# Kernel optimization log

Measured on AMD Instinct MI355X. Metric: run time of the kernel, lower is better.

Reference implementation:

```python
import jax, jax.numpy as jnp
import numpy as np

B, N, D, H, C = 8, 1024, 1024, 8, 1
S = 32            # sqrt(D // C): per-patch spatial map side
HD = D // H       # head dim = 128
SCALE = HD ** -0.5
BN_EPS = 1e-3     # Keras BatchNormalization default epsilon


def setup_inputs() -> dict:
    key = jax.random.key(0)
    ks = jax.random.split(key, 7)
    std = 0.02  # matches tf.random_normal_initializer(0.0, 0.02)
    return {
        "x": jax.random.normal(ks[0], (B, N, D), jnp.float32),
        "qw": jax.random.normal(ks[1], (3, 3, C, C), jnp.float32) * std,
        "kw": jax.random.normal(ks[2], (3, 3, C, C), jnp.float32) * std,
        "vw": jax.random.normal(ks[3], (3, 3, C, C), jnp.float32) * std,
        "reatten_w": jax.random.normal(ks[4], (N, N), jnp.float32) / np.float32(np.sqrt(N)),
        "reatten_b": jnp.zeros((N,), jnp.float32),
        "bn_gamma": jnp.ones((N,), jnp.float32),
        "bn_beta": jnp.zeros((N,), jnp.float32),
        "proj_w": jax.random.normal(ks[5], (D, D), jnp.float32) / np.float32(np.sqrt(D)),
        "proj_b": jnp.zeros((D,), jnp.float32),
    }


def _conv_qkv(x, w):
    # unflatten: [B, N, D] -> [B*N, S, S, C]; map_fn over batch with a shared
    # conv == one conv with B*N as batch dim. 3x3 SAME, no bias, exact GELU.
    xm = x.reshape(B * N, S, S, C)
    y = jax.lax.conv_general_dilated(
        xm, w, window_strides=(1, 1), padding='SAME',
        dimension_numbers=('NHWC', 'HWIO', 'NHWC'))
    y = jax.nn.gelu(y, approximate=False)
    # reshape to heads: [B, N, H, HD] -> [B, H, N, HD]
    return y.reshape(B, N, H, HD).transpose(0, 2, 1, 3)


def reference(x, qw, kw, vw, reatten_w, reatten_b, bn_gamma, bn_beta, proj_w, proj_b):
    q = _conv_qkv(x, qw)
    k = _conv_qkv(x, kw)
    v = _conv_qkv(x, vw)

    attn = jax.nn.softmax(jnp.einsum('bhid,bhjd->bhij', q, k) * SCALE, axis=-1)
    # re-attention: 1x1 conv over last (key) axis + BN (inference: mean=0, var=1)
    attn = jnp.einsum('bhic,cj->bhij', attn, reatten_w) + reatten_b
    attn = attn * (bn_gamma / jnp.sqrt(jnp.float32(1.0) + BN_EPS)) + bn_beta
    # reatten_scale = 1.0 (transform_scale=False)

    out = jnp.einsum('bhij,bhjd->bhid', attn, v)
    out = out.transpose(0, 2, 1, 3).reshape(B, N, D)
    out = out @ proj_w + proj_b
    return (out, attn)
```

## Files before the change

kernel.cpp:

```cpp
#include <hip/hip_runtime.h>
#include <hip/hip_bf16.h>

typedef __attribute__((ext_vector_type(8))) short short8;
typedef __attribute__((ext_vector_type(4))) float f32x4;

__device__ __forceinline__ void gload_lds16(const void* g, void* l) {
    __builtin_amdgcn_global_load_lds(
        (const __attribute__((address_space(1))) void*)g,
        (__attribute__((address_space(3))) void*)l, 16, 0, 0);
}

__device__ __forceinline__ float gelu_exact(float x) {
    return 0.5f * x * (1.0f + erff(x * 0.70710678118654752f));
}
__device__ __forceinline__ unsigned short f2b_raw(float f) {
    __hip_bfloat16 h = __float2bfloat16(f);
    return *reinterpret_cast<unsigned short*>(&h);
}
__device__ __forceinline__ float tofloat(float f) { return f; }
__device__ __forceinline__ float tofloat(__hip_bfloat16 h) { return __bfloat162float(h); }

__global__ __launch_bounds__(256) void conv_qkv(
    const float* __restrict__ x,
    const float* __restrict__ qw, const float* __restrict__ kw, const float* __restrict__ vw,
    __hip_bfloat16* __restrict__ qb, __hip_bfloat16* __restrict__ kb, __hip_bfloat16* __restrict__ vb)
{
    __shared__ float img[1024];
    const int bid = blockIdx.x;
    const int b = bid >> 10, n = bid & 1023;
    const float* xr = x + (long)bid * 1024;
    for (int i = threadIdx.x; i < 1024; i += 256) img[i] = xr[i];
    __syncthreads();

    float wq[9], wk[9], wv[9];
    #pragma unroll
    for (int i = 0; i < 9; ++i) { wq[i] = qw[i]; wk[i] = kw[i]; wv[i] = vw[i]; }

    for (int q = 0; q < 4; ++q) {
        const int p = q * 256 + threadIdx.x;
        const int r = p >> 5, c = p & 31;
        float sq = 0.f, sk = 0.f, sv = 0.f;
        #pragma unroll
        for (int dy = 0; dy < 3; ++dy) {
            const int rr = r + dy - 1;
            if (rr < 0 || rr > 31) continue;
            #pragma unroll
            for (int dx = 0; dx < 3; ++dx) {
                const int cc = c + dx - 1;
                if (cc < 0 || cc > 31) continue;
                const float px = img[rr * 32 + cc];
                sq += px * wq[dy * 3 + dx];
                sk += px * wk[dy * 3 + dx];
                sv += px * wv[dy * 3 + dx];
            }
        }
        sq = gelu_exact(sq); sk = gelu_exact(sk); sv = gelu_exact(sv);
        const int h = p >> 7, d = p & 127;
        const long off = ((long)(b * 8 + h) * 1024 + n) * 128 + d;
        qb[off] = __float2bfloat16(sq);
        kb[off] = __float2bfloat16(sk);
        vb[off] = __float2bfloat16(sv);
    }
}

template <typename Tin>
__global__ __launch_bounds__(256) void transpose_cast(
    const Tin* __restrict__ in, __hip_bfloat16* __restrict__ out,
    int R, int Cc, long inz, long outz)
{
    __shared__ float tile[32][33];
    const long z = blockIdx.z;
    const int c0 = blockIdx.x * 32, r0 = blockIdx.y * 32;
    const int tx = threadIdx.x & 31, ty = threadIdx.x >> 5;
    const Tin* ip = in + z * inz;
    #pragma unroll
    for (int i = 0; i < 32; i += 8)
        tile[ty + i][tx] = tofloat(ip[(long)(r0 + ty + i) * Cc + (c0 + tx)]);
    __syncthreads();
    __hip_bfloat16* op = out + z * outz;
    #pragma unroll
    for (int i = 0; i < 32; i += 8)
        op[(long)(c0 + ty + i) * R + (r0 + tx)] = __float2bfloat16(tile[tx][ty + i]);
}

__global__ __launch_bounds__(256, 2) void qk_softmax(
    const __hip_bfloat16* __restrict__ qb, const __hip_bfloat16* __restrict__ kb,
    __hip_bfloat16* __restrict__ Pun, float* __restrict__ linv)
{
    __shared__ __align__(16) char smem[74240];
    char* As = smem;
    char* Bs = smem + 32768;
    __hip_bfloat16* pbuf = (__hip_bfloat16*)(smem + 65536);
    float* lred = (float*)(smem + 65536);

    const int tid = threadIdx.x;
    const int rt = blockIdx.x, z = blockIdx.y;
    const char* Ag = (const char*)(qb + ((long)z * 1024 + rt * 128) * 128);
    const char* Bg = (const char*)(kb + (long)z * 1024 * 128);

    int gsrc[8], pphys[8];
    #pragma unroll
    for (int i = 0; i < 8; ++i) {
        const int p = i * 4096 + tid * 16;
        const int L = p ^ (((p >> 8) & 7) << 4);
        pphys[i] = p; gsrc[i] = L;
    }
    auto STAGE = [&](const char* gb, char* lb) {
        #pragma unroll
        for (int i = 0; i < 8; ++i) gload_lds16(gb + gsrc[i], lb + pphys[i]);
    };
    auto LD8 = [&](const char* buf, int L) -> short8 {
        const int ph = L ^ (((L >> 8) & 7) << 4);
        return *(const short8*)(buf + ph);
    };

    const int lane = tid & 63, wave = tid >> 6;
    const int wr = (wave >> 1) * 64, wc = (wave & 1) * 64;
    const int fr = lane & 15, kl = lane >> 4;

    STAGE(Ag, As);
    STAGE(Bg, Bs);
    __syncthreads();

    short8 af[4][4];
    #pragma unroll
    for (int m = 0; m < 4; ++m)
        #pragma unroll
        for (int kk = 0; kk < 4; ++kk)
            af[m][kk] = LD8(As, (wr + m * 16 + fr) * 256 + (kl * 8 + kk * 32) * 2);

    float lacc[4][4];
    #pragma unroll
    for (int m = 0; m < 4; ++m)
        #pragma unroll
        for (int r = 0; r < 4; ++r) lacc[m][r] = 0.f;

    const float SCALE = 0.08838834764831843f;

    for (int c = 0; c < 8; ++c) {
        f32x4 acc[4][4];
        #pragma unroll
        for (int m = 0; m < 4; ++m)
            #pragma unroll
            for (int n = 0; n < 4; ++n) acc[m][n] = (f32x4){0.f, 0.f, 0.f, 0.f};

        #pragma unroll
        for (int kk = 0; kk < 4; ++kk) {
            short8 bf[4];
            #pragma unroll
            for (int n = 0; n < 4; ++n)
                bf[n] = LD8(Bs, (wc + n * 16 + fr) * 256 + (kl * 8 + kk * 32) * 2);
            #pragma unroll
            for (int m = 0; m < 4; ++m)
                #pragma unroll
                for (int n = 0; n < 4; ++n)
                    acc[m][n] = __builtin_amdgcn_mfma_f32_16x16x32_bf16(af[m][kk], bf[n], acc[m][n], 0, 0, 0);
        }

        #pragma unroll
        for (int m = 0; m < 4; ++m) {
            #pragma unroll
            for (int n = 0; n < 4; ++n)
                #pragma unroll
                for (int r = 0; r < 4; ++r)
                    acc[m][n][r] = __expf(acc[m][n][r] * SCALE);
            #pragma unroll
            for (int r = 0; r < 4; ++r)
                lacc[m][r] += (acc[m][0][r] + acc[m][1][r]) + (acc[m][2][r] + acc[m][3][r]);
        }

        #pragma unroll
        for (int q2 = 0; q2 < 4; ++q2) {
            if ((wave >> 1) == (q2 >> 1)) {
                #pragma unroll
                for (int mm = 0; mm < 2; ++mm) {
                    const int m = (q2 & 1) * 2 + mm;
                    const int lr0 = m * 16 + kl * 4 - (q2 & 1) * 32;
                    #pragma unroll
                    for (int n = 0; n < 4; ++n)
                        #pragma unroll
                        for (int r = 0; r < 4; ++r)
                            pbuf[(lr0 + r) * 136 + wc + n * 16 + fr] = __float2bfloat16(acc[m][n][r]);
                }
            }
            __syncthreads();
            #pragma unroll
            for (int p = 0; p < 2; ++p) {
                const int idx = (tid + p * 256) * 8;
                const int row = idx >> 7, col = idx & 127;
                short8 s = *(const short8*)&pbuf[row * 136 + col];
                __builtin_nontemporal_store(s,
                    (short8*)&Pun[((long)z * 1024 + rt * 128 + q2 * 32 + row) * 1024 + c * 128 + col]);
            }
            __syncthreads();
        }

        if (c < 7) {
            STAGE(Bg + (c + 1) * 32768, Bs);
            __syncthreads();
        }
    }

    #pragma unroll
    for (int m = 0; m < 4; ++m)
        #pragma unroll
        for (int r = 0; r < 4; ++r) {
            float v = lacc[m][r];
            v += __shfl_xor(v, 1); v += __shfl_xor(v, 2);
            v += __shfl_xor(v, 4); v += __shfl_xor(v, 8);
            lacc[m][r] = v;
        }
    __syncthreads();
    if (fr == 0) {
        #pragma unroll
        for (int m = 0; m < 4; ++m)
            #pragma unroll
            for (int r = 0; r < 4; ++r)
                lred[(wr + m * 16 + kl * 4 + r) * 2 + (wave & 1)] = lacc[m][r];
    }
    __syncthreads();
    if (tid < 128) {
        const float s = lred[tid * 2] + lred[tid * 2 + 1];
        linv[(long)z * 1024 + rt * 128 + tid] = 1.0f / s;
    }
}

__global__ __launch_bounds__(512, 2) void gemm_reatten_256(
    const __hip_bfloat16* __restrict__ Sall, const __hip_bfloat16* __restrict__ Wt,
    float* __restrict__ Cout, __hip_bfloat16* __restrict__ C2out,
    const float* __restrict__ bg, const float* __restrict__ rb, const float* __restrict__ bb,
    const float* __restrict__ linv)
{
    __shared__ __align__(16) char smem[131072];
    char* ldsA = smem;
    char* ldsB = smem + 65536;

    const int tid = threadIdx.x;
    const int z = blockIdx.z, tileM = blockIdx.x, tileN = blockIdx.y;
    const char* Ab = (const char*)(Sall + (long)z * 1048576 + (long)tileM * 256 * 1024);
    const char* Bb = (const char*)(Wt + (long)tileN * 256 * 1024);

    int grow[2], goff[2], pphys[2];
    #pragma unroll
    for (int i = 0; i < 2; ++i) {
        const int p = i * 8192 + tid * 16;
        const int l = p ^ (((p >> 7) & 3) << 4);
        pphys[i] = p; grow[i] = l >> 6; goff[i] = l & 63;
    }
    auto STAGE = [&](const char* gb, char* lb, int kt) {
        #pragma unroll
        for (int i = 0; i < 2; ++i)
            gload_lds16(gb + (long)grow[i] * 2048 + kt * 64 + goff[i], lb + pphys[i]);
    };

    const int lane = tid & 63, wid = tid >> 6;
    const int wrM = wid >> 2, wcn = wid & 3;
    const int fr = lane & 15, kl = lane >> 4;
    const int frbase = fr * 64 + kl * 16;

    auto LD8 = [&](const char* buf, int L) -> short8 {
        const int ph = L ^ (((L >> 7) & 3) << 4);
        return *(const short8*)(buf + ph);
    };

    f32x4 acc[8][4];
    #pragma unroll
    for (int m = 0; m < 8; ++m)
        #pragma unroll
        for (int n = 0; n < 4; ++n) acc[m][n] = (f32x4){0.f, 0.f, 0.f, 0.f};

    STAGE(Ab, ldsA, 0);          STAGE(Bb, ldsB, 0);
    STAGE(Ab, ldsA + 16384, 1);  STAGE(Bb, ldsB + 16384, 1);
    asm volatile("s_waitcnt vmcnt(4)" ::: "memory");
    __builtin_amdgcn_sched_barrier(0);
    __builtin_amdgcn_s_barrier();
    __builtin_amdgcn_sched_barrier(0);

    #pragma unroll 1
    for (int t = 0; t < 32; ++t) {
        char* bufA = ldsA + (t & 3) * 16384;
        char* bufB = ldsB + (t & 3) * 16384;
        const int t2 = t + 2;
        char* nA = ldsA + (t2 & 3) * 16384;
        char* nB = ldsB + (t2 & 3) * 16384;

        short8 bf[4], af[4], ag[4];
        #pragma unroll
        for (int n = 0; n < 4; ++n) bf[n] = LD8(bufB, ((wcn * 64 + n * 16) * 64) + frbase);
        #pragma unroll
        for (int j = 0; j < 4; ++j) af[j] = LD8(bufA, ((wrM * 128 + j * 16) * 64) + frbase);
        if (t2 < 32) STAGE(Ab, nA, t2);
        __builtin_amdgcn_s_setprio(1);
        #pragma unroll
        for (int j = 0; j < 4; ++j)
            #pragma unroll
            for (int n = 0; n < 4; ++n)
                acc[j][n] = __builtin_amdgcn_mfma_f32_16x16x32_bf16(af[j], bf[n], acc[j][n], 0, 0, 0);
        __builtin_amdgcn_s_setprio(0);

        #pragma unroll
        for (int j = 0; j < 4; ++j) ag[j] = LD8(bufA, ((wrM * 128 + 64 + j * 16) * 64) + frbase);
        if (t2 < 32) STAGE(Bb, nB, t2);
        __builtin_amdgcn_s_setprio(1);
        #pragma unroll
        for (int j = 0; j < 4; ++j)
            #pragma unroll
            for (int n = 0; n < 4; ++n)
                acc[4 + j][n] = __builtin_amdgcn_mfma_f32_16x16x32_bf16(ag[j], bf[n], acc[4 + j][n], 0, 0, 0);
        __builtin_amdgcn_s_setprio(0);

        if (t < 30)       { asm volatile("s_waitcnt vmcnt(4)" ::: "memory"); }
        else if (t == 30) { asm volatile("s_waitcnt vmcnt(0)" ::: "memory"); }
        __builtin_amdgcn_sched_barrier(0);
        __builtin_amdgcn_s_barrier();
        __builtin_amdgcn_sched_barrier(0);
    }

    __syncthreads();
    float* cbuf = (float*)smem;
    const float bninv = rsqrtf(1.0f + 1e-3f);
    float alpha[4], addv[4];
    #pragma unroll
    for (int n = 0; n < 4; ++n) {
        const int col = tileN * 256 + wcn * 64 + n * 16 + fr;
        const float g = bg[col];
        alpha[n] = g * bninv;
        addv[n] = rb[col] * alpha[n] + bb[col];
    }
    const float* linvz = linv + (long)z * 1024 + tileM * 256 + wrM * 128 + kl * 4;
    f32x4 lr[8];
    #pragma unroll
    for (int mf = 0; mf < 8; ++mf) lr[mf] = *(const f32x4*)(linvz + mf * 16);

    const int srow = tid >> 3, cseg = (tid & 7) * 4, c8 = (tid & 7) * 8;
    #pragma unroll
    for (int c = 0; c < 4; ++c) {
        if (wrM == (c >> 1)) {
            #pragma unroll
            for (int j = 0; j < 4; ++j) {
                const int mf = (c & 1) * 4 + j;
                const int lrow0 = j * 16 + kl * 4;
                #pragma unroll
                for (int n = 0; n < 4; ++n)
                    #pragma unroll
                    for (int r = 0; r < 4; ++r)
                        cbuf[(lrow0 + r) * 260 + wcn * 64 + n * 16 + fr] =
                            acc[mf][n][r] * (lr[mf][r] * alpha[n]) + addv[n];
            }
        }
        __syncthreads();
        const long gro = (long)(tileM * 256 + c * 64 + srow);
        float* gp = Cout + (long)z * 1048576 + gro * 1024 + tileN * 256;
        #pragma unroll
        for (int i = 0; i < 8; ++i) {
            f32x4 v = *(const f32x4*)&cbuf[srow * 260 + cseg + i * 32];
            __builtin_nontemporal_store(v, (f32x4*)(gp + cseg + i * 32));
        }
        __hip_bfloat16* gp2 = C2out + (long)z * 1048576 + gro * 1024 + tileN * 256;
        #pragma unroll
        for (int i = 0; i < 4; ++i) {
            const float* src = &cbuf[srow * 260 + c8 + i * 64];
            f32x4 v0 = *(const f32x4*)src;
            f32x4 v1 = *(const f32x4*)(src + 4);
            short8 s;
            #pragma unroll
            for (int k = 0; k < 4; ++k) {
                s[k] = (short)f2b_raw(v0[k]);
                s[k + 4] = (short)f2b_raw(v1[k]);
            }
            *(short8*)(gp2 + c8 + i * 64) = s;
        }
        __syncthreads();
    }
}

template <int MODE>
__global__ __launch_bounds__(256) void gemm_nt(
    const __hip_bfloat16* __restrict__ Aall, const __hip_bfloat16* __restrict__ Ball,
    void* __restrict__ Call, int K,
    long sAz, long sBz, long sCz,
    const float* __restrict__ e0)
{
    constexpr bool OF32 = (MODE == 3);

    __shared__ __align__(16) char smem[32 * 132 * 4];
    short* As = (short*)smem;
    short* Bs = (short*)(smem + 8192);
    float* cbuf = (float*)smem;

    const int tid = threadIdx.x;
    const int z = blockIdx.z;
    const int tileM = blockIdx.x, tileN = blockIdx.y;

    const short* Aw = (const short*)Aall + sAz * z + (long)tileM * 128 * K;
    const short* Bw = (const short*)Ball + sBz * z + (long)tileN * 128 * K;

    const int r0s = tid >> 2, k0s = (tid & 3) * 8;
    const int r1s = r0s + 64;

    f32x4 acc[4][4];
    #pragma unroll
    for (int m = 0; m < 4; ++m)
        #pragma unroll
        for (int n = 0; n < 4; ++n) acc[m][n] = (f32x4){0.f, 0.f, 0.f, 0.f};

    const int lane = tid & 63;
    const int wave = tid >> 6;
    const int wr = (wave >> 1) * 64, wc = (wave & 1) * 64;
    const int fr = lane & 15;
    const int kb = (lane >> 4) * 8;

    const int nk = K >> 5;
    for (int kt = 0; kt < nk; ++kt) {
        __syncthreads();
        gload_lds16(Aw + (long)r0s * K + kt * 32 + k0s, &As[tid * 8]);
        gload_lds16(Aw + (long)r1s * K + kt * 32 + k0s, &As[(tid + 256) * 8]);
        gload_lds16(Bw + (long)r0s * K + kt * 32 + k0s, &Bs[tid * 8]);
        gload_lds16(Bw + (long)r1s * K + kt * 32 + k0s, &Bs[(tid + 256) * 8]);
        __syncthreads();

        short8 af[4], bf[4];
        #pragma unroll
        for (int m = 0; m < 4; ++m) af[m] = *(const short8*)&As[(wr + m * 16 + fr) * 32 + kb];
        #pragma unroll
        for (int n = 0; n < 4; ++n) bf[n] = *(const short8*)&Bs[(wc + n * 16 + fr) * 32 + kb];
        #pragma unroll
        for (int m = 0; m < 4; ++m)
            #pragma unroll
            for (int n = 0; n < 4; ++n)
                acc[m][n] = __builtin_amdgcn_mfma_f32_16x16x32_bf16(af[m], bf[n], acc[m][n], 0, 0, 0);
    }

    long cbase;
    if (MODE == 2) cbase = (long)(z >> 3) * 1048576 + (long)(z & 7) * 128;
    else           cbase = sCz * z;

    float addv[4];
    #pragma unroll
    for (int n = 0; n < 4; ++n) {
        const int col = tileN * 128 + wc + n * 16 + fr;
        addv[n] = (MODE == 3) ? e0[col] : 0.f;
    }

    __syncthreads();
    #pragma unroll
    for (int q = 0; q < 4; ++q) {
        if ((wave >> 1) == (q >> 1)) {
            #pragma unroll
            for (int mm = 0; mm < 2; ++mm) {
                const int m = (q & 1) * 2 + mm;
                const int lr0 = m * 16 + (lane >> 4) * 4 - (q & 1) * 32;
                #pragma unroll
                for (int n = 0; n < 4; ++n)
                    #pragma unroll
                    for (int r = 0; r < 4; ++r)
                        cbuf[(lr0 + r) * 132 + wc + n * 16 + fr] = acc[m][n][r] + addv[n];
            }
        }
        __syncthreads();
        const long growbase = (long)tileM * 128 + q * 32;
        if constexpr (OF32) {
            float* Cg = (float*)Call + cbase;
            #pragma unroll
            for (int pass = 0; pass < 4; ++pass) {
                const int idx = (tid + pass * 256) * 4;
                const int row = idx >> 7, col = idx & 127;
                f32x4 v = *(const f32x4*)&cbuf[row * 132 + col];
                __builtin_nontemporal_store(v,
                    (f32x4*)&Cg[(growbase + row) * 1024 + tileN * 128 + col]);
            }
        } else {
            __hip_bfloat16* Cg = (__hip_bfloat16*)Call + cbase;
            #pragma unroll
            for (int pass = 0; pass < 2; ++pass) {
                const int idx = (tid + pass * 256) * 8;
                const int row = idx >> 7, col = idx & 127;
                const float* src = &cbuf[row * 132 + col];
                f32x4 v0 = *(const f32x4*)src;
                f32x4 v1 = *(const f32x4*)(src + 4);
                short8 s;
                #pragma unroll
                for (int i = 0; i < 4; ++i) {
                    s[i] = (short)f2b_raw(v0[i]);
                    s[i + 4] = (short)f2b_raw(v1[i]);
                }
                *(short8*)&Cg[(growbase + row) * 1024 + tileN * 128 + col] = s;
            }
        }
        __syncthreads();
    }
}

extern "C" void kernel_launch(void* const* d_in, const int* in_sizes, int n_in,
                              void* d_out, int out_size, void* d_ws, size_t ws_size,
                              hipStream_t stream)
{
    const float* x  = (const float*)d_in[0];
    const float* qw = (const float*)d_in[1];
    const float* kw = (const float*)d_in[2];
    const float* vw = (const float*)d_in[3];
    const float* rw = (const float*)d_in[4];
    const float* rb = (const float*)d_in[5];
    const float* bg = (const float*)d_in[6];
    const float* bb = (const float*)d_in[7];
    const float* pw = (const float*)d_in[8];
    const float* pb = (const float*)d_in[9];

    float* outF  = (float*)d_out;
    float* attnF = outF + 8388608;

    char* w = (char*)d_ws;
    __hip_bfloat16* qb    = (__hip_bfloat16*)w; w += 16777216;
    __hip_bfloat16* kb    = (__hip_bfloat16*)w; w += 16777216;
    __hip_bfloat16* vb    = (__hip_bfloat16*)w; w += 16777216;
    __hip_bfloat16* vt    = (__hip_bfloat16*)w; w += 16777216;
    __hip_bfloat16* Wt    = (__hip_bfloat16*)w; w += 2097152;
    __hip_bfloat16* pWt   = (__hip_bfloat16*)w; w += 2097152;
    __hip_bfloat16* o2    = (__hip_bfloat16*)w; w += 16777216;
    float*          linv  = (float*)w;          w += 262144;
    __hip_bfloat16* Pun   = (__hip_bfloat16*)w; w += 134217728;
    __hip_bfloat16* attnb = (__hip_bfloat16*)w; w += 134217728;

    conv_qkv<<<8192, 256, 0, stream>>>(x, qw, kw, vw, qb, kb, vb);
    transpose_cast<float><<<dim3(32, 32, 1), 256, 0, stream>>>(rw, Wt, 1024, 1024, 0, 0);
    transpose_cast<float><<<dim3(32, 32, 1), 256, 0, stream>>>(pw, pWt, 1024, 1024, 0, 0);
    transpose_cast<__hip_bfloat16><<<dim3(4, 32, 64), 256, 0, stream>>>(vb, vt, 1024, 128, 131072, 131072);

    qk_softmax<<<dim3(8, 64), 256, 0, stream>>>(qb, kb, Pun, linv);
    gemm_reatten_256<<<dim3(4, 4, 64), 512, 0, stream>>>(Pun, Wt, attnF, attnb, bg, rb, bb, linv);
    gemm_nt<2><<<dim3(8, 1, 64), 256, 0, stream>>>(
        attnb, vt, o2, 1024, 1048576, 131072, 0, nullptr);
    gemm_nt<3><<<dim3(64, 8, 1), 256, 0, stream>>>(
        o2, pWt, outF, 1024, 0, 0, 0, pb);
}
```

Before: 371.9 us.

## Drop bf16 attention copy; attn@V GEMM reads fp32 attn and converts in-kernel

```diff
diff --git a/kernel.cpp b/kernel.cpp
--- a/kernel.cpp
+++ b/kernel.cpp
@@ -184,6 +184,7 @@
                 }
             }
             __syncthreads();
+            if (q2 == 0 && c < 7) STAGE(Bg + (c + 1) * 32768, Bs);
             #pragma unroll
             for (int p = 0; p < 2; ++p) {
                 const int idx = (tid + p * 256) * 8;
@@ -194,11 +195,6 @@
             }
             __syncthreads();
         }
-
-        if (c < 7) {
-            STAGE(Bg + (c + 1) * 32768, Bs);
-            __syncthreads();
-        }
     }
 
     #pragma unroll
@@ -227,7 +223,7 @@
 
 __global__ __launch_bounds__(512, 2) void gemm_reatten_256(
     const __hip_bfloat16* __restrict__ Sall, const __hip_bfloat16* __restrict__ Wt,
-    float* __restrict__ Cout, __hip_bfloat16* __restrict__ C2out,
+    float* __restrict__ Cout,
     const float* __restrict__ bg, const float* __restrict__ rb, const float* __restrict__ bb,
     const float* __restrict__ linv)
 {
@@ -332,7 +328,7 @@
     #pragma unroll
     for (int mf = 0; mf < 8; ++mf) lr[mf] = *(const f32x4*)(linvz + mf * 16);
 
-    const int srow = tid >> 3, cseg = (tid & 7) * 4, c8 = (tid & 7) * 8;
+    const int srow = tid >> 3, cseg = (tid & 7) * 4;
     #pragma unroll
     for (int c = 0; c < 4; ++c) {
         if (wrM == (c >> 1)) {
@@ -356,31 +352,18 @@
             f32x4 v = *(const f32x4*)&cbuf[srow * 260 + cseg + i * 32];
             __builtin_nontemporal_store(v, (f32x4*)(gp + cseg + i * 32));
         }
-        __hip_bfloat16* gp2 = C2out + (long)z * 1048576 + gro * 1024 + tileN * 256;
-        #pragma unroll
-        for (int i = 0; i < 4; ++i) {
-            const float* src = &cbuf[srow * 260 + c8 + i * 64];
-            f32x4 v0 = *(const f32x4*)src;
-            f32x4 v1 = *(const f32x4*)(src + 4);
-            short8 s;
-            #pragma unroll
-            for (int k = 0; k < 4; ++k) {
-                s[k] = (short)f2b_raw(v0[k]);
-                s[k + 4] = (short)f2b_raw(v1[k]);
-            }
-            *(short8*)(gp2 + c8 + i * 64) = s;
-        }
         __syncthreads();
     }
 }
 
 template <int MODE>
 __global__ __launch_bounds__(256) void gemm_nt(
-    const __hip_bfloat16* __restrict__ Aall, const __hip_bfloat16* __restrict__ Ball,
+    const void* __restrict__ Aall, const __hip_bfloat16* __restrict__ Ball,
     void* __restrict__ Call, int K,
     long sAz, long sBz, long sCz,
     const float* __restrict__ e0)
 {
+    constexpr bool AF32 = (MODE == 2);
     constexpr bool OF32 = (MODE == 3);
 
     __shared__ __align__(16) char smem[32 * 132 * 4];
@@ -392,7 +375,10 @@
     const int z = blockIdx.z;
     const int tileM = blockIdx.x, tileN = blockIdx.y;
 
-    const short* Aw = (const short*)Aall + sAz * z + (long)tileM * 128 * K;
+    const short* AwB = nullptr;
+    const float* AwF = nullptr;
+    if constexpr (AF32) AwF = (const float*)Aall + sAz * z + (long)tileM * 128 * K;
+    else                AwB = (const short*)Aall + sAz * z + (long)tileM * 128 * K;
     const short* Bw = (const short*)Ball + sBz * z + (long)tileN * 128 * K;
 
     const int r0s = tid >> 2, k0s = (tid & 3) * 8;
@@ -412,12 +398,33 @@
 
     const int nk = K >> 5;
     for (int kt = 0; kt < nk; ++kt) {
-        __syncthreads();
-        gload_lds16(Aw + (long)r0s * K + kt * 32 + k0s, &As[tid * 8]);
-        gload_lds16(Aw + (long)r1s * K + kt * 32 + k0s, &As[(tid + 256) * 8]);
-        gload_lds16(Bw + (long)r0s * K + kt * 32 + k0s, &Bs[tid * 8]);
-        gload_lds16(Bw + (long)r1s * K + kt * 32 + k0s, &Bs[(tid + 256) * 8]);
-        __syncthreads();
+        if constexpr (AF32) {
+            const float* Ak0 = AwF + (long)r0s * K + kt * 32 + k0s;
+            const float* Ak1 = AwF + (long)r1s * K + kt * 32 + k0s;
+            f32x4 a00 = *(const f32x4*)Ak0;
+            f32x4 a01 = *(const f32x4*)(Ak0 + 4);
+            f32x4 a10 = *(const f32x4*)Ak1;
+            f32x4 a11 = *(const f32x4*)(Ak1 + 4);
+            __syncthreads();
+            short8 s0, s1;
+            #pragma unroll
+            for (int i = 0; i < 4; ++i) {
+                s0[i] = (short)f2b_raw(a00[i]); s0[i + 4] = (short)f2b_raw(a01[i]);
+                s1[i] = (short)f2b_raw(a10[i]); s1[i + 4] = (short)f2b_raw(a11[i]);
+            }
+            *(short8*)&As[tid * 8] = s0;
+            *(short8*)&As[(tid + 256) * 8] = s1;
+            gload_lds16(Bw + (long)r0s * K + kt * 32 + k0s, &Bs[tid * 8]);
+            gload_lds16(Bw + (long)r1s * K + kt * 32 + k0s, &Bs[(tid + 256) * 8]);
+            __syncthreads();
+        } else {
+            __syncthreads();
+            gload_lds16(AwB + (long)r0s * K + kt * 32 + k0s, &As[tid * 8]);
+            gload_lds16(AwB + (long)r1s * K + kt * 32 + k0s, &As[(tid + 256) * 8]);
+            gload_lds16(Bw + (long)r0s * K + kt * 32 + k0s, &Bs[tid * 8]);
+            gload_lds16(Bw + (long)r1s * K + kt * 32 + k0s, &Bs[(tid + 256) * 8]);
+            __syncthreads();
+        }
 
         short8 af[4], bf[4];
         #pragma unroll
@@ -467,7 +474,8 @@
                 const int row = idx >> 7, col = idx & 127;
                 f32x4 v = *(const f32x4*)&cbuf[row * 132 + col];
                 __builtin_nontemporal_store(v,
-                    (f32x4*)&Cg[(growbase + row) * 1024 + tileN * 128 + col]);
+                    (f32x4*)&((float*)Call)[cbase + (growbase + row) * 1024 + tileN * 128 + col]);
+                (void)Cg;
             }
         } else {
             __hip_bfloat16* Cg = (__hip_bfloat16*)Call + cbase;
@@ -519,7 +527,6 @@
     __hip_bfloat16* o2    = (__hip_bfloat16*)w; w += 16777216;
     float*          linv  = (float*)w;          w += 262144;
     __hip_bfloat16* Pun   = (__hip_bfloat16*)w; w += 134217728;
-    __hip_bfloat16* attnb = (__hip_bfloat16*)w; w += 134217728;
 
     conv_qkv<<<8192, 256, 0, stream>>>(x, qw, kw, vw, qb, kb, vb);
     transpose_cast<float><<<dim3(32, 32, 1), 256, 0, stream>>>(rw, Wt, 1024, 1024, 0, 0);
@@ -527,9 +534,9 @@
     transpose_cast<__hip_bfloat16><<<dim3(4, 32, 64), 256, 0, stream>>>(vb, vt, 1024, 128, 131072, 131072);
 
     qk_softmax<<<dim3(8, 64), 256, 0, stream>>>(qb, kb, Pun, linv);
-    gemm_reatten_256<<<dim3(4, 4, 64), 512, 0, stream>>>(Pun, Wt, attnF, attnb, bg, rb, bb, linv);
+    gemm_reatten_256<<<dim3(4, 4, 64), 512, 0, stream>>>(Pun, Wt, attnF, bg, rb, bb, linv);
     gemm_nt<2><<<dim3(8, 1, 64), 256, 0, stream>>>(
-        attnb, vt, o2, 1024, 1048576, 131072, 0, nullptr);
+        attnF, vt, o2, 1024, 1048576, 131072, 0, nullptr);
     gemm_nt<3><<<dim3(64, 8, 1), 256, 0, stream>>>(
         o2, pWt, outF, 1024, 0, 0, 0, pb);
 }
```

Result: slower. 397.7 us (+6.9%).
